# Optimization experiments

Hardware: AMD Instinct MI355X
Metric: run time of the kernel (lower is better)

The kernel has to match this reference:

```python
import jax, jax.numpy as jnp
import numpy as np
from jax import lax

B, T, NI = 1024, 16, 11

def skew(v):  # [...,3,1] -> [...,3,3]
    x, y, z = v[..., 0, 0], v[..., 1, 0], v[..., 2, 0]
    o = jnp.zeros_like(x)
    return jnp.stack([jnp.stack([o, -z, y], -1),
                      jnp.stack([z, o, -x], -1),
                      jnp.stack([-y, x, o], -1)], -2)

def exp_SO3(phi):  # [...,3,1] -> [...,3,3] (Rodrigues, safe small-angle)
    t2 = jnp.sum(phi * phi, axis=(-2, -1))[..., None, None]
    small = t2 < 1e-8
    t2s = jnp.where(small, 1.0, t2)
    t = jnp.sqrt(t2s)
    A = jnp.where(small, 1.0 - t2 / 6.0, jnp.sin(t) / t)
    Bc = jnp.where(small, 0.5 - t2 / 24.0, (1.0 - jnp.cos(t)) / t2s)
    K = skew(phi)
    return jnp.eye(3, dtype=phi.dtype) + A * K + Bc * (K @ K)

def log_SO3(C):  # [...,3,3] -> [...,3,1]
    tr = jnp.trace(C, axis1=-2, axis2=-1)[..., None, None]
    c = jnp.clip((tr - 1.0) * 0.5, -1.0 + 1e-7, 1.0 - 1e-7)
    t = jnp.arccos(c)
    small = t < 1e-4
    s = jnp.where(small, 1.0, jnp.sin(t))
    coef = jnp.where(small, 0.5 + t * t / 12.0, t / (2.0 * s))
    S = coef * (C - jnp.swapaxes(C, -1, -2))
    return jnp.stack([S[..., 2, 1], S[..., 0, 2], S[..., 1, 0]], -1)[..., None]

def J_left_inv(phi):  # inverse left Jacobian of SO(3)
    t2 = jnp.sum(phi * phi, axis=(-2, -1))[..., None, None]
    small = t2 < 1e-8
    t2s = jnp.where(small, 1.0, t2)
    t = jnp.sqrt(t2s)
    coef = jnp.where(small, 1.0 / 12.0,
                     1.0 / t2s - (1.0 + jnp.cos(t)) / (2.0 * t * jnp.sin(t)))
    K = skew(phi)
    return jnp.eye(3, dtype=phi.dtype) - 0.5 * K + coef * (K @ K)

def decode(s):
    b = s.shape[0]
    return (s[:, 0:3].reshape(b, 3, 1), s[:, 3:12].reshape(b, 3, 3),
            s[:, 12:15].reshape(b, 3, 1), s[:, 15:18].reshape(b, 3, 1),
            s[:, 18:21].reshape(b, 3, 1), s[:, 21:24].reshape(b, 3, 1),
            s[:, 24].reshape(b, 1, 1))

def encode(g, C, r, v, bw, ba, lambd):
    b = g.shape[0]
    return jnp.concatenate([g.reshape(b, 3), C.reshape(b, 9), r.reshape(b, 3),
                            v.reshape(b, 3), bw.reshape(b, 3), ba.reshape(b, 3),
                            lambd.reshape(b, 1)], -1)

def force_sym(M):
    u = jnp.triu(M)
    return u + jnp.swapaxes(u, -1, -2) * (1.0 - jnp.eye(M.shape[-1], dtype=M.dtype))

def predict_one_step(t_acc, C_acc, r_acc, v_acc, dt, g_k, v_k, bw_k, ba_k, covar, gyro, accel, Rimu):
    b = dt.shape[0]
    dt2 = dt * dt
    w = gyro - bw_k
    w_sk = skew(w)
    C_T = jnp.swapaxes(C_acc, -1, -2)
    a = accel - ba_k
    v = C_T @ (v_k - g_k * t_acc + v_acc)
    v_sk = skew(v)
    I3 = jnp.eye(3, dtype=dt.dtype)
    E = exp_SO3(dt * w)
    E_T = jnp.swapaxes(E, -1, -2)
    F = jnp.zeros((b, 19, 19), dt.dtype)
    F = F.at[:, 3:6, 3:6].set(-w_sk)
    F = F.at[:, 3:6, 12:15].set(-I3)
    F = F.at[:, 6:9, 3:6].set(-(C_acc @ v_sk))
    F = F.at[:, 6:9, 9:12].set(C_acc)
    F = F.at[:, 9:12, 0:3].set(-C_T)
    F = F.at[:, 9:12, 3:6].set(-skew(C_T @ g_k))
    F = F.at[:, 9:12, 9:12].set(-w_sk)
    F = F.at[:, 9:12, 12:15].set(-v_sk)
    F = F.at[:, 9:12, 15:18].set(-I3)
    G = jnp.zeros((b, 19, 12), dt.dtype)
    G = G.at[:, 3:6, 0:3].set(-I3)
    G = G.at[:, 9:12, 0:3].set(-v_sk)
    G = G.at[:, 9:12, 6:9].set(-I3)
    G = G.at[:, 12:15, 3:6].set(I3)
    G = G.at[:, 15:18, 9:12].set(I3)
    Phi = jnp.eye(19, dtype=dt.dtype) + F * dt + 0.5 * (F @ F) * dt2
    Phi = Phi.at[:, 6:9, 12:15].set(0.0)
    Phi = Phi.at[:, 3:6, 3:6].set(E_T)
    Phi = Phi.at[:, 9:12, 9:12].set(E_T)
    PhiG = Phi @ G
    Q = (PhiG @ Rimu @ jnp.swapaxes(PhiG, -1, -2)) * dt
    covar = force_sym(Phi @ covar @ jnp.swapaxes(Phi, -1, -2) + Q)
    r_acc = r_acc + v_acc * dt + 0.5 * (C_acc @ (dt2 * a))
    v_acc = v_acc + C_acc @ (dt * a)
    C_acc = C_acc @ E
    t_acc = t_acc + dt
    return t_acc, C_acc, r_acc, v_acc, covar

def predict(imu_meas, Rimu, prev_state, prev_covar):
    b = imu_meas.shape[0]
    dtype = prev_covar.dtype
    g_k, _, _, v_k, bw_k, ba_k, lambd = decode(prev_state)
    u = jnp.array([1.0] * 3 + [0.0] * 6 + [1.0] * 10, dtype)
    covar = prev_covar * (u[:, None] * u[None, :])  # U P U^T with diagonal U
    t = imu_meas[..., 0]
    gyro = imu_meas[..., 1:4][..., None]
    accel = imu_meas[..., 4:7][..., None]
    dt = (t[:, 1:] - t[:, :-1])[..., None, None]
    init = (jnp.zeros((b, 1, 1), dtype),
            jnp.tile(jnp.eye(3, dtype=dtype), (b, 1, 1)),
            jnp.zeros((b, 3, 1), dtype), jnp.zeros((b, 3, 1), dtype), covar)
    xs = (jnp.swapaxes(dt, 0, 1), jnp.swapaxes(gyro[:, :-1], 0, 1), jnp.swapaxes(accel[:, :-1], 0, 1))
    def step(c, x):
        t_acc, C_acc, r_acc, v_acc, cov = c
        dt_, gy, ac = x
        return predict_one_step(t_acc, C_acc, r_acc, v_acc, dt_, g_k, v_k, bw_k, ba_k, cov, gy, ac, Rimu), None
    (t_acc, C_acc, r_acc, v_acc, cov), _ = lax.scan(step, init, xs)
    pred_state = encode(g_k, C_acc,
                        v_k * t_acc - 0.5 * g_k * t_acc * t_acc + r_acc,
                        jnp.swapaxes(C_acc, -1, -2) @ (v_k - g_k * t_acc + v_acc),
                        bw_k, ba_k, lambd)
    return pred_state, cov

def update(pred_state, pred_covar, vis_meas, vis_meas_covar):
    b = pred_state.shape[0]
    dtype = pred_state.dtype
    g_p, C_p, r_p, v_p, bw_p, ba_p, l_p = decode(pred_state)
    phi = log_SO3(C_p)
    residual = jnp.concatenate([vis_meas[:, 0:3] - phi, vis_meas[:, 3:6] - l_p * r_p], 1)
    H = jnp.zeros((b, 6, 19), dtype)
    H = H.at[:, 0:3, 3:6].set(-J_left_inv(-phi))
    H = H.at[:, 3:6, 6:9].set(-jnp.eye(3, dtype=dtype) * l_p)
    H = H.at[:, 3:6, 18:19].set(-r_p)
    H = -H
    H_T = jnp.swapaxes(H, -1, -2)
    S = H @ pred_covar @ H_T + vis_meas_covar
    K = pred_covar @ H_T @ jnp.linalg.inv(S)
    e = K @ residual
    est_covar = (jnp.eye(19, dtype=dtype) - K @ H) @ pred_covar
    est_state = encode(g_p + e[:, 0:3], C_p @ exp_SO3(e[:, 3:6]), r_p + e[:, 6:9],
                       v_p + e[:, 9:12], bw_p + e[:, 12:15], ba_p + e[:, 15:18],
                       l_p + e[:, 18:19])
    return est_state, est_covar

def composition(prev_pose, est_state, est_covar):
    b = est_state.shape[0]
    dtype = est_state.dtype
    g, C, r, v, bw, ba, lambd = decode(est_state)
    C_T = jnp.swapaxes(C, -1, -2)
    pose = jnp.tile(jnp.eye(4, dtype=dtype), (b, 1, 1))
    pose = pose.at[:, 0:3, 0:3].set(C_T @ prev_pose[:, 0:3, 0:3])
    pose = pose.at[:, 0:3, 3:4].set(C_T @ (prev_pose[:, 0:3, 3:4] - r))
    new_g = C_T @ g
    new_state = encode(new_g, C, r, v, bw, ba, lambd)
    U = jnp.tile(jnp.eye(19, dtype=dtype), (b, 1, 1))
    U = U.at[:, 0:3, 0:3].set(C_T)
    U = U.at[:, 0:3, 3:6].set(skew(new_g))
    new_covar = force_sym(U @ est_covar @ jnp.swapaxes(U, -1, -2))
    return pose, new_state, new_covar

def setup_inputs() -> dict:
    key = jax.random.key(0)
    k1, k2, k3 = jax.random.split(key, 3)
    dtype = jnp.float32
    times = jnp.broadcast_to(jnp.arange(NI, dtype=dtype) * 0.01, (B, T, NI))
    gyro = jax.random.normal(k1, (B, T, NI, 3), dtype) * 0.05
    accel = jax.random.normal(k2, (B, T, NI, 3), dtype) * 0.1
    imu_data = jnp.concatenate([times[..., None], gyro, accel], -1)  # [B,T,NI,7]
    imu_noise_covar = jnp.eye(12, dtype=dtype) * 1e-4
    prev_pose = jnp.tile(jnp.eye(4, dtype=dtype), (B, 1, 1))
    g0 = jnp.array([0.0, 0.0, 9.81], dtype)
    C0 = jnp.eye(3, dtype=dtype).reshape(9)
    prev_state = jnp.broadcast_to(
        jnp.concatenate([g0, C0, jnp.zeros(12, dtype), jnp.ones(1, dtype)]), (B, 25))
    prev_covar = jnp.tile(jnp.eye(19, dtype=dtype) * 1e-2, (B, 1, 1))
    vis_meas = jax.random.normal(k3, (B, T, 6, 1), dtype) * 0.01
    vis_meas_covar = jnp.tile(jnp.eye(6, dtype=dtype) * 1e-2, (B, T, 1, 1))
    T_imu_cam = jnp.tile(jnp.eye(4, dtype=dtype), (B, 1, 1))
    return dict(imu_data=imu_data, imu_noise_covar=imu_noise_covar, prev_pose=prev_pose,
                prev_state=prev_state, prev_covar=prev_covar, vis_meas=vis_meas,
                vis_meas_covar=vis_meas_covar, T_imu_cam=T_imu_cam)

def reference(imu_data, imu_noise_covar, prev_pose, prev_state, prev_covar, vis_meas, vis_meas_covar, T_imu_cam):
    num_timesteps = vis_meas.shape[1]
    poses, states, covars = [prev_pose], [prev_state], [prev_covar]
    for k in range(num_timesteps):
        ps, pc = predict(imu_data[:, k], imu_noise_covar, states[-1], covars[-1])
        es, ec = update(ps, pc, vis_meas[:, k], vis_meas_covar[:, k])
        npo, ns, nc = composition(poses[-1], es, ec)
        poses.append(npo); states.append(ns); covars.append(nc)
    return (jnp.stack(poses, 1), jnp.stack(states, 1), jnp.stack(covars, 1))
```

## Files before the change

kernel.cpp:

```cpp
#include <hip/hip_runtime.h>

#define NB 1024
#define NT 16
#define NIM 11
#define PIT 20
#define NTH 256
#define TPF 128

struct __align__(16) SharedBlob {
    float P0[19*PIT];
    float P1[19*PIT];
    float A9[9*PIT];
    float Dall[10][9*PIT];
    float Wsall[10][9*12];
    float Wu[19*12];
    float Mu[19*12];
    float T[3*PIT];
    float Rd[12];
    float sqRd[12];
    float Aug[2][84];
    float E[20];
    float dts[12];
    unsigned short tri[192];
};

__device__ __forceinline__ float sel3(int i, float a, float b, float c){
    return i==0 ? a : (i==1 ? b : c);
}
__device__ __forceinline__ void skew3(float x, float y, float z, float K[9]) {
    K[0]=0.f;  K[1]=-z;   K[2]=y;
    K[3]=z;    K[4]=0.f;  K[5]=-x;
    K[6]=-y;   K[7]=x;    K[8]=0.f;
}
__device__ __forceinline__ void mm3(const float A[9], const float Bm[9], float C[9]) {
#pragma unroll
    for (int i=0;i<3;i++)
#pragma unroll
        for (int j=0;j<3;j++)
            C[i*3+j] = A[i*3+0]*Bm[0+j] + A[i*3+1]*Bm[3+j] + A[i*3+2]*Bm[6+j];
}
__device__ __forceinline__ void exp_SO3f(float p0, float p1, float p2, float R[9]) {
    float t2 = p0*p0+p1*p1+p2*p2;
    bool sm = t2 < 1e-8f;
    float t2s = sm ? 1.0f : t2;
    float t = sqrtf(t2s);
    float sn, cs; __sincosf(t, &sn, &cs);
    float A = sm ? (1.0f - t2*(1.0f/6.0f)) : (sn/t);
    float Bc = sm ? (0.5f - t2*(1.0f/24.0f)) : ((1.0f - cs)/t2s);
    float K[9]; skew3(p0,p1,p2,K);
    float K2[9]; mm3(K,K,K2);
#pragma unroll
    for (int i=0;i<9;i++) R[i] = A*K[i] + Bc*K2[i];
    R[0]+=1.f; R[4]+=1.f; R[8]+=1.f;
}
__device__ __forceinline__ void log_SO3(const float C[9], float p[3]) {
    float tr = C[0]+C[4]+C[8];
    float c = (tr-1.0f)*0.5f;
    c = fminf(fmaxf(c, -1.0f+1e-7f), 1.0f-1e-7f);
    float t = acosf(c);
    bool sm = t < 1e-4f;
    float s = sm ? 1.0f : sinf(t);
    float coef = sm ? (0.5f + t*t*(1.0f/12.0f)) : (t/(2.0f*s));
    p[0] = coef*(C[7]-C[5]);
    p[1] = coef*(C[2]-C[6]);
    p[2] = coef*(C[3]-C[1]);
}
__device__ __forceinline__ void J_left_inv(const float p[3], float J[9]) {
    float t2 = p[0]*p[0]+p[1]*p[1]+p[2]*p[2];
    bool sm = t2 < 1e-8f;
    float t2s = sm ? 1.0f : t2;
    float t = sqrtf(t2s);
    float coef = sm ? (1.0f/12.0f) : (1.0f/t2s - (1.0f+cosf(t))/(2.0f*t*sinf(t)));
    float K[9]; skew3(p[0],p[1],p[2],K);
    float K2[9]; mm3(K,K,K2);
#pragma unroll
    for (int i=0;i<9;i++) J[i] = -0.5f*K[i] + coef*K2[i];
    J[0]+=1.f; J[4]+=1.f; J[8]+=1.f;
}
__device__ __forceinline__ float dot19_rr(const float* a, const float* b){
    const float4* a4=(const float4*)a;
    const float4* b4=(const float4*)b;
    float s=0.f;
#pragma unroll
    for (int q=0;q<4;q++){
        float4 x=a4[q], y=b4[q];
        s += x.x*y.x + x.y*y.y + x.z*y.z + x.w*y.w;
    }
    s += a[16]*b[16]+a[17]*b[17]+a[18]*b[18];
    return s;
}
__device__ __forceinline__ float dot12_rr(const float* a, const float* b){
    const float4* a4=(const float4*)a;
    const float4* b4=(const float4*)b;
    float s=0.f;
#pragma unroll
    for (int q=0;q<3;q++){
        float4 x=a4[q], y=b4[q];
        s += x.x*y.x + x.y*y.y + x.z*y.z + x.w*y.w;
    }
    return s;
}

__global__ void __launch_bounds__(NTH, 2) kf_kernel(
    const float* __restrict__ imu_data,
    const float* __restrict__ Rimu,
    const float* __restrict__ prev_pose,
    const float* __restrict__ prev_state,
    const float* __restrict__ prev_covar,
    const float* __restrict__ vis_meas,
    const float* __restrict__ vis_covar,
    float* __restrict__ out_poses,
    float* __restrict__ out_states,
    float* __restrict__ out_covars)
{
    __shared__ SharedBlob SS[2];
    const int tid = threadIdx.x;
    const int f   = tid >> 7;
    const int t   = tid & (TPF-1);
    const int b   = blockIdx.x*2 + f;
    SharedBlob& S = SS[f];
    const int w = t >> 6;
    const int l = t & 63;

    const float* pcv = prev_covar + (size_t)b*361;
    for (int e=t;e<361;e+=TPF){
        float v = pcv[e];
        int i=e/19, j=e%19;
        bool msk = (i>=3&&i<9)||(j>=3&&j<9);
        S.P0[i*PIT + j] = msk ? 0.f : v;
        out_covars[((size_t)b*17)*361 + e] = v;
    }
    for (int e=t;e<10*9*PIT;e+=TPF) S.Dall[0][e] = 0.f;
    if (t<12){ float rv = Rimu[t*12+t]; S.Rd[t]=rv; S.sqRd[t]=sqrtf(rv); }
    if (t<16) out_poses[((size_t)b*17)*16 + t] = prev_pose[(size_t)b*16+t];
    if (t<25) out_states[((size_t)b*17)*25 + t] = prev_state[(size_t)b*25+t];
    for (int e=t;e<190;e+=TPF){
        int i=0, rem=e;
        while (rem >= 19-i){ rem -= 19-i; i++; }
        S.tri[e] = (unsigned short)((i<<5)|(i+rem));
    }

    const float* st = prev_state + (size_t)b*25;
    float g0=st[0], g1=st[1], g2=st[2];
    float vk0=st[15], vk1=st[16], vk2=st[17];
    float bw0=st[18], bw1=st[19], bw2=st[20];
    float ba0=st[21], ba1=st[22], ba2=st[23];
    float lam=st[24];
    const float* pp = prev_pose + (size_t)b*16;
    float pR[9] = {pp[0],pp[1],pp[2], pp[4],pp[5],pp[6], pp[8],pp[9],pp[10]};
    float pT0=pp[3], pT1=pp[7], pT2=pp[11];

    __syncthreads();

    for (int k=0;k<NT;k++){
        float Cc[9] = {1,0,0, 0,1,0, 0,0,1};
        float ra0=0,ra1=0,ra2=0, va0=0,va1=0,va2=0, tac=0;
        const float* imu = imu_data + ((size_t)b*NT + k)*NIM*7;

        for (int s=0;s<NIM-1;s++){
            const float* m0 = imu + s*7;
            float dt = m0[7] - m0[0];
            float w0=m0[1]-bw0, w1=m0[2]-bw1, w2=m0[3]-bw2;
            float a0=m0[4]-ba0, a1=m0[5]-ba1, a2=m0[6]-ba2;
            float u0=vk0-g0*tac+va0, u1=vk1-g1*tac+va1, u2=vk2-g2*tac+va2;
            float vv0=Cc[0]*u0+Cc[3]*u1+Cc[6]*u2;
            float vv1=Cc[1]*u0+Cc[4]*u1+Cc[7]*u2;
            float vv2=Cc[2]*u0+Cc[5]*u1+Cc[8]*u2;
            float ct0=Cc[0]*g0+Cc[3]*g1+Cc[6]*g2;
            float ct1=Cc[1]*g0+Cc[4]*g1+Cc[7]*g2;
            float ct2=Cc[2]*g0+Cc[5]*g1+Cc[8]*g2;
            float Em[9]; exp_SO3f(dt*w0, dt*w1, dt*w2, Em);
            float hdt2 = 0.5f*dt*dt;

            if (t<27){
                int r=t/9, ii=(t%9)/3, jj=t%3;
                float dij = (ii==jj)?1.f:0.f;
                int o = ii*PIT + jj;
                float* Dp = S.Dall[s];
                if (r==0){
                    float eJ0=sel3(jj,Em[0],Em[3],Em[6]), eJ1=sel3(jj,Em[1],Em[4],Em[7]), eJ2=sel3(jj,Em[2],Em[5],Em[8]);
                    float EmTIJ = sel3(ii,eJ0,eJ1,eJ2);
                    float wcJ0=sel3(jj,0.f,-w2,w1), wcJ1=sel3(jj,w2,0.f,-w0), wcJ2=sel3(jj,-w1,w0,0.f);
                    float wskIJ = sel3(ii,wcJ0,wcJ1,wcJ2);
                    Dp[o+3]  = EmTIJ - dij;
                    Dp[o+12] = -dt*dij + hdt2*wskIJ;
                } else if (r==1){
                    float cI0=sel3(ii,Cc[0],Cc[3],Cc[6]), cI1=sel3(ii,Cc[1],Cc[4],Cc[7]), cI2=sel3(ii,Cc[2],Cc[5],Cc[8]);
                    float cJ0=sel3(jj,Cc[0],Cc[3],Cc[6]), cJ1=sel3(jj,Cc[1],Cc[4],Cc[7]), cJ2=sel3(jj,Cc[2],Cc[5],Cc[8]);
                    float ccJ0=sel3(jj,Cc[0],Cc[1],Cc[2]), ccJ1=sel3(jj,Cc[3],Cc[4],Cc[5]), ccJ2=sel3(jj,Cc[6],Cc[7],Cc[8]);
                    float CIJ = sel3(ii,ccJ0,ccJ1,ccJ2);
                    float vcJ0=sel3(jj,0.f,-vv2,vv1), vcJ1=sel3(jj,vv2,0.f,-vv0), vcJ2=sel3(jj,-vv1,vv0,0.f);
                    float tcJ0=sel3(jj,0.f,-ct2,ct1), tcJ1=sel3(jj,ct2,0.f,-ct0), tcJ2=sel3(jj,-ct1,ct0,0.f);
                    float wcJ0=sel3(jj,0.f,-w2,w1), wcJ1=sel3(jj,w2,0.f,-w0), wcJ2=sel3(jj,-w1,w0,0.f);
                    float CCtIJ  = cI0*cJ0 + cI1*cJ1 + cI2*cJ2;
                    float CvskIJ = cI0*vcJ0 + cI1*vcJ1 + cI2*vcJ2;
                    float Cv0 =  cI1*vv2 - cI2*vv1;
                    float Cv1 = -cI0*vv2 + cI2*vv0;
                    float Cv2 =  cI0*vv1 - cI1*vv0;
                    float CvwIJ = Cv0*wcJ0 + Cv1*wcJ1 + Cv2*wcJ2;
                    float CctIJ = cI0*tcJ0 + cI1*tcJ1 + cI2*tcJ2;
                    float CwIJ  = cI0*wcJ0 + cI1*wcJ1 + cI2*wcJ2;
                    Dp[3*PIT + o + 0]  = -hdt2*CCtIJ;
                    Dp[3*PIT + o + 3]  = -dt*CvskIJ + hdt2*(CvwIJ - CctIJ);
                    Dp[3*PIT + o + 9]  =  dt*CIJ - hdt2*CwIJ;
                    Dp[3*PIT + o + 15] = -hdt2*CIJ;
                } else {
                    float cJ0=sel3(jj,Cc[0],Cc[3],Cc[6]), cJ1=sel3(jj,Cc[1],Cc[4],Cc[7]), cJ2=sel3(jj,Cc[2],Cc[5],Cc[8]);
                    float CTIJ = sel3(ii,cJ0,cJ1,cJ2);
                    float eJ0=sel3(jj,Em[0],Em[3],Em[6]), eJ1=sel3(jj,Em[1],Em[4],Em[7]), eJ2=sel3(jj,Em[2],Em[5],Em[8]);
                    float EmTIJ = sel3(ii,eJ0,eJ1,eJ2);
                    float wrI0=sel3(ii,0.f,w2,-w1), wrI1=sel3(ii,-w2,0.f,w0), wrI2=sel3(ii,w1,-w0,0.f);
                    float wcJ0=sel3(jj,0.f,-w2,w1), wcJ1=sel3(jj,w2,0.f,-w0), wcJ2=sel3(jj,-w1,w0,0.f);
                    float wskIJ = sel3(ii,wcJ0,wcJ1,wcJ2);
                    float vcJ0=sel3(jj,0.f,-vv2,vv1), vcJ1=sel3(jj,vv2,0.f,-vv0), vcJ2=sel3(jj,-vv1,vv0,0.f);
                    float vskIJ = sel3(ii,vcJ0,vcJ1,vcJ2);
                    float trI0=sel3(ii,0.f,ct2,-ct1), trI1=sel3(ii,-ct2,0.f,ct0), trI2=sel3(ii,ct1,-ct0,0.f);
                    float tcJ0=sel3(jj,0.f,-ct2,ct1), tcJ1=sel3(jj,ct2,0.f,-ct0), tcJ2=sel3(jj,-ct1,ct0,0.f);
                    float ctskIJ = sel3(ii,tcJ0,tcJ1,tcJ2);
                    float wCtIJ = wrI0*cJ0 + wrI1*cJ1 + wrI2*cJ2;
                    float ctwIJ = trI0*wcJ0 + trI1*wcJ1 + trI2*wcJ2;
                    float wctIJ = wrI0*tcJ0 + wrI1*tcJ1 + wrI2*tcJ2;
                    float wvIJ  = wrI0*vcJ0 + wrI1*vcJ1 + wrI2*vcJ2;
                    Dp[6*PIT + o + 0]  = -dt*CTIJ + hdt2*wCtIJ;
                    Dp[6*PIT + o + 3]  = -dt*ctskIJ + hdt2*(ctwIJ + wctIJ);
                    Dp[6*PIT + o + 9]  = EmTIJ - dij;
                    Dp[6*PIT + o + 12] = -dt*vskIJ + hdt2*(ctskIJ + wvIJ);
                    Dp[6*PIT + o + 15] = -dt*dij + hdt2*wskIJ;
                }
            }
            if (t==3) S.dts[s] = dt;
            if (w==0){
                __builtin_amdgcn_wave_barrier();
                asm volatile("s_waitcnt lgkmcnt(0)" ::: "memory");
                __builtin_amdgcn_wave_barrier();
                float* Wp = S.Wsall[s];
                const float* Dp2 = S.Dall[s];
                for (int e=l;e<108;e+=64){
                    int i=e/12, j=e%12;
                    const float* Dr = &Dp2[i*PIT];
                    int ri = 3+i;
                    float val;
                    if (j<3){
                        float v0j = sel3(j, 0.f, -vv2,  vv1);
                        float v1j = sel3(j, vv2,  0.f, -vv0);
                        float v2j = sel3(j,-vv1,  vv0,  0.f);
                        val = -((ri==3+j)?1.f:0.f) - Dr[3+j]
                              - (((ri==9 )?1.f:0.f)+Dr[9 ])*v0j
                              - (((ri==10)?1.f:0.f)+Dr[10])*v1j
                              - (((ri==11)?1.f:0.f)+Dr[11])*v2j;
                    } else if (j<6) val = Dr[9+j];
                    else if (j<9) val = -(((ri==j+3)?1.f:0.f) + Dr[j+3]);
                    else val = Dr[6+j];
                    Wp[i*12+j] = val * S.sqRd[j];
                }
            }

            float d2 = dt*dt;
            float e0=d2*a0, e1=d2*a1, e2=d2*a2;
            ra0 += va0*dt + 0.5f*(Cc[0]*e0+Cc[1]*e1+Cc[2]*e2);
            ra1 += va1*dt + 0.5f*(Cc[3]*e0+Cc[4]*e1+Cc[5]*e2);
            ra2 += va2*dt + 0.5f*(Cc[6]*e0+Cc[7]*e1+Cc[8]*e2);
            float da0=dt*a0, da1=dt*a1, da2=dt*a2;
            va0 += Cc[0]*da0+Cc[1]*da1+Cc[2]*da2;
            va1 += Cc[3]*da0+Cc[4]*da1+Cc[5]*da2;
            va2 += Cc[6]*da0+Cc[7]*da1+Cc[8]*da2;
            float Cn[9]; mm3(Cc, Em, Cn);
#pragma unroll
            for (int q=0;q<9;q++) Cc[q]=Cn[q];
            tac += dt;
        }
        __syncthreads();

        for (int s=0;s<NIM-1;s++){
            float* Pc = (s&1) ? S.P1 : S.P0;
            float* Pn = (s&1) ? S.P0 : S.P1;
            const float* Ds = S.Dall[s];
            const float* Wss = S.Wsall[s];
            float dt = S.dts[s];

            int aBeg = (w==0)?0:57, aEnd = (w==0)?57:171;
            for (int e=aBeg+l;e<aEnd;e+=64){
                int i=e/19, j=e%19;
                const float* Dr = &Ds[i*PIT];
                float s2 = Pc[(3+i)*PIT+j]
                         + Dr[0]*Pc[0*PIT+j]+Dr[1]*Pc[1*PIT+j]+Dr[2]*Pc[2*PIT+j]
                         + Dr[3]*Pc[3*PIT+j]+Dr[4]*Pc[4*PIT+j]+Dr[5]*Pc[5*PIT+j]
                         + Dr[9]*Pc[9*PIT+j]+Dr[10]*Pc[10*PIT+j]+Dr[11]*Pc[11*PIT+j]
                         + Dr[12]*Pc[12*PIT+j]+Dr[13]*Pc[13*PIT+j]+Dr[14]*Pc[14*PIT+j]
                         + Dr[15]*Pc[15*PIT+j]+Dr[16]*Pc[16*PIT+j]+Dr[17]*Pc[17*PIT+j];
                S.A9[i*PIT+j]=s2;
            }
            __builtin_amdgcn_wave_barrier();
            asm volatile("s_waitcnt lgkmcnt(0)" ::: "memory");
            __builtin_amdgcn_wave_barrier();

            int tBase = (w==0)?0:99, tCnt = (w==0)?99:91;
            for (int e2=l;e2<tCnt;e2+=64){
                int tt=S.tri[tBase+e2]; int i=tt>>5, j=tt&31;
                const float* Ai = (i>=3 && i<12) ? &S.A9[(i-3)*PIT] : &Pc[i*PIT];
                float val = Ai[j];
                if (j>=3 && j<12) val += dot19_rr(Ai, &Ds[(j-3)*PIT]);
                if (i>=3){
                    if (j<12) val += dt*dot12_rr(&Wss[(i-3)*12], &Wss[(j-3)*12]);
                    else if (i<12){
                        if (j<15) val += dt*Wss[(i-3)*12 + (j-9)]*S.sqRd[j-9];
                        else if (j<18) val += dt*Wss[(i-3)*12 + (j-6)]*S.sqRd[j-6];
                    } else if (i==j){
                        if (i<15) val += dt*S.Rd[i-9];
                        else if (i<18) val += dt*S.Rd[i-6];
                    }
                }
                Pn[i*PIT+j]=val; Pn[j*PIT+i]=val;
            }
            __syncthreads();
        }

        float t2a = tac*tac;
        float rp0 = vk0*tac - 0.5f*g0*t2a + ra0;
        float rp1 = vk1*tac - 0.5f*g1*t2a + ra1;
        float rp2 = vk2*tac - 0.5f*g2*t2a + ra2;
        float u0=vk0-g0*tac+va0, u1=vk1-g1*tac+va1, u2=vk2-g2*tac+va2;
        float vpr0=Cc[0]*u0+Cc[3]*u1+Cc[6]*u2;
        float vpr1=Cc[1]*u0+Cc[4]*u1+Cc[7]*u2;
        float vpr2=Cc[2]*u0+Cc[5]*u1+Cc[8]*u2;

        float phi[3]; log_SO3(Cc, phi);
        float nphi[3]={-phi[0],-phi[1],-phi[2]};
        float Jli[9]; J_left_inv(nphi, Jli);
        const float* vm = vis_meas + ((size_t)b*NT+k)*6;
        float res0=vm[0]-phi[0], res1=vm[1]-phi[1], res2=vm[2]-phi[2];
        float res3=vm[3]-lam*rp0, res4=vm[4]-lam*rp1, res5=vm[5]-lam*rp2;

        if (t<114){
            int i=t/6, j=t%6;
            float val;
            if (j<3){
                float jr0 = sel3(j, Jli[0], Jli[3], Jli[6]);
                float jr1 = sel3(j, Jli[1], Jli[4], Jli[7]);
                float jr2 = sel3(j, Jli[2], Jli[5], Jli[8]);
                val = S.P0[i*PIT+3]*jr0 + S.P0[i*PIT+4]*jr1 + S.P0[i*PIT+5]*jr2;
            } else {
                float rsel = sel3(j-3, rp0, rp1, rp2);
                val = lam*S.P0[i*PIT+6+(j-3)] + rsel*S.P0[i*PIT+18];
            }
            S.Wu[i*12+j]=val;
        }
        __syncthreads();
        const float* vmc = vis_covar + ((size_t)b*NT+k)*36;
        if (t<84){
            int i=t/14, c=t%14;
            float val;
            if (c<6){
                float hp;
                if (i<3){
                    float jr0 = sel3(i, Jli[0], Jli[3], Jli[6]);
                    float jr1 = sel3(i, Jli[1], Jli[4], Jli[7]);
                    float jr2 = sel3(i, Jli[2], Jli[5], Jli[8]);
                    hp = jr0*S.Wu[3*12+c]+jr1*S.Wu[4*12+c]+jr2*S.Wu[5*12+c];
                } else {
                    float rsel = sel3(i-3, rp0, rp1, rp2);
                    hp = lam*S.Wu[(3+i)*12+c] + rsel*S.Wu[18*12+c];
                }
                val = hp + vmc[i*6+c];
            } else val = ((c-6)==i)?1.f:0.f;
            S.Aug[0][i*14+c]=val;
        }
        __syncthreads();
        if (t<64){
            int i0=t/14, c0=t%14;
            int e1=t+64, i1=e1/14, c1=e1%14;
            bool h1 = e1<84;
            int cur=0;
#pragma unroll
            for (int kk=0;kk<6;kk++){
                const float* Ac = S.Aug[cur];
                float* An = S.Aug[cur^1];
                float rpv = 1.0f/Ac[kk*14+kk];
                float piv0 = Ac[kk*14+c0]*rpv;
                float nv0 = (i0==kk)? piv0 : (Ac[i0*14+c0] - Ac[i0*14+kk]*piv0);
                float nv1 = 0.f;
                if (h1){
                    float piv1 = Ac[kk*14+c1]*rpv;
                    nv1 = (i1==kk)? piv1 : (Ac[i1*14+c1] - Ac[i1*14+kk]*piv1);
                }
                An[i0*14+c0]=nv0;
                if (h1) An[i1*14+c1]=nv1;
                cur^=1;
                __builtin_amdgcn_wave_barrier();
            }
        }
        __syncthreads();
        if (t<114){
            int i=t/6, j=t%6;
            float s2=0.f;
#pragma unroll
            for (int m=0;m<6;m++) s2 += S.Wu[i*12+m]*S.Aug[0][m*14+6+j];
            S.Mu[i*12+j]=s2;
        }
        __syncthreads();
        for (int e=t;e<133;e+=TPF){
            int i=e/7, c=e%7;
            float val;
            if (c<3){
                float jc0 = sel3(c, Jli[0], Jli[1], Jli[2]);
                float jc1 = sel3(c, Jli[3], Jli[4], Jli[5]);
                float jc2 = sel3(c, Jli[6], Jli[7], Jli[8]);
                val = S.Mu[i*12+0]*jc0 + S.Mu[i*12+1]*jc1 + S.Mu[i*12+2]*jc2;
            }
            else if (c<6) val = S.Mu[i*12+c]*lam;
            else val = S.Mu[i*12+3]*rp0 + S.Mu[i*12+4]*rp1 + S.Mu[i*12+5]*rp2;
            S.Wu[i*12+c]=val;
        }
        if (t<19){
            S.E[t] = S.Mu[t*12+0]*res0 + S.Mu[t*12+1]*res1 + S.Mu[t*12+2]*res2
                   + S.Mu[t*12+3]*res3 + S.Mu[t*12+4]*res4 + S.Mu[t*12+5]*res5;
        }
        __syncthreads();
        for (int e=t;e<361;e+=TPF){
            int i=e/19, j=e%19;
            float s2 = S.P0[i*PIT+j];
#pragma unroll
            for (int c=0;c<6;c++) s2 -= S.Wu[i*12+c]*S.P0[(3+c)*PIT+j];
            s2 -= S.Wu[i*12+6]*S.P0[18*PIT+j];
            S.P1[i*PIT+j]=s2;
        }
        float ev[19];
#pragma unroll
        for (int q=0;q<19;q++) ev[q]=S.E[q];
        g0+=ev[0]; g1+=ev[1]; g2+=ev[2];
        float dE[9]; exp_SO3f(ev[3], ev[4], ev[5], dE);
        float Ce[9]; mm3(Cc,dE,Ce);
        float re0=rp0+ev[6], re1=rp1+ev[7], re2=rp2+ev[8];
        float vE0=vpr0+ev[9], vE1=vpr1+ev[10], vE2=vpr2+ev[11];
        bw0+=ev[12]; bw1+=ev[13]; bw2+=ev[14];
        ba0+=ev[15]; ba1+=ev[16]; ba2+=ev[17];
        lam+=ev[18];
        float gn0=Ce[0]*g0+Ce[3]*g1+Ce[6]*g2;
        float gn1=Ce[1]*g0+Ce[4]*g1+Ce[7]*g2;
        float gn2=Ce[2]*g0+Ce[5]*g1+Ce[8]*g2;
        float Rn[9];
#pragma unroll
        for (int i=0;i<3;i++)
#pragma unroll
            for (int j=0;j<3;j++)
                Rn[i*3+j] = Ce[0*3+i]*pR[0*3+j] + Ce[1*3+i]*pR[1*3+j] + Ce[2*3+i]*pR[2*3+j];
        float dv0=pT0-re0, dv1=pT1-re1, dv2=pT2-re2;
        float Tn0=Ce[0]*dv0+Ce[3]*dv1+Ce[6]*dv2;
        float Tn1=Ce[1]*dv0+Ce[4]*dv1+Ce[7]*dv2;
        float Tn2=Ce[2]*dv0+Ce[5]*dv1+Ce[8]*dv2;
        __syncthreads();
        if (t<57){
            int i=t/19, j=t%19;
            float c0 = sel3(i, Ce[0], Ce[1], Ce[2]);
            float c1 = sel3(i, Ce[3], Ce[4], Ce[5]);
            float c2 = sel3(i, Ce[6], Ce[7], Ce[8]);
            float gs0 = sel3(i, 0.f,  gn2, -gn1);
            float gs1 = sel3(i, -gn2, 0.f,  gn0);
            float gs2 = sel3(i, gn1, -gn0,  0.f);
            float val = c0*S.P1[0*PIT+j] + c1*S.P1[1*PIT+j] + c2*S.P1[2*PIT+j]
                      + gs0*S.P1[3*PIT+j] + gs1*S.P1[4*PIT+j] + gs2*S.P1[5*PIT+j];
            S.T[i*PIT+j]=val;
        }
        __syncthreads();
        size_t obase = (size_t)b*17 + (size_t)(k+1);
        for (int e=t;e<190;e+=TPF){
            int tt=S.tri[e]; int i=tt>>5, j=tt&31;
            float val;
            if (j<3){
                float c0 = sel3(j, Ce[0], Ce[1], Ce[2]);
                float c1 = sel3(j, Ce[3], Ce[4], Ce[5]);
                float c2 = sel3(j, Ce[6], Ce[7], Ce[8]);
                float gs0 = sel3(j, 0.f,  gn2, -gn1);
                float gs1 = sel3(j, -gn2, 0.f,  gn0);
                float gs2 = sel3(j, gn1, -gn0,  0.f);
                val = S.T[i*PIT+0]*c0 + S.T[i*PIT+1]*c1 + S.T[i*PIT+2]*c2
                    + S.T[i*PIT+3]*gs0 + S.T[i*PIT+4]*gs1 + S.T[i*PIT+5]*gs2;
            } else {
                val = (i<3) ? S.T[i*PIT+j] : S.P1[i*PIT+j];
            }
            bool msk = (i>=3&&i<9)||(j>=3&&j<9);
            float pv = msk ? 0.f : val;
            S.P0[i*PIT+j]=pv; S.P0[j*PIT+i]=pv;
            out_covars[obase*361 + i*19 + j] = val;
            if (i!=j) out_covars[obase*361 + j*19 + i] = val;
        }
        if (t==0){
            float* po = out_poses + obase*16;
            po[0]=Rn[0]; po[1]=Rn[1]; po[2]=Rn[2];  po[3]=Tn0;
            po[4]=Rn[3]; po[5]=Rn[4]; po[6]=Rn[5];  po[7]=Tn1;
            po[8]=Rn[6]; po[9]=Rn[7]; po[10]=Rn[8]; po[11]=Tn2;
            po[12]=0.f; po[13]=0.f; po[14]=0.f; po[15]=1.f;
            float* so = out_states + obase*25;
            so[0]=gn0; so[1]=gn1; so[2]=gn2;
#pragma unroll
            for (int q=0;q<9;q++) so[3+q]=Ce[q];
            so[12]=re0; so[13]=re1; so[14]=re2;
            so[15]=vE0; so[16]=vE1; so[17]=vE2;
            so[18]=bw0; so[19]=bw1; so[20]=bw2;
            so[21]=ba0; so[22]=ba1; so[23]=ba2;
            so[24]=lam;
        }
        g0=gn0; g1=gn1; g2=gn2;
        vk0=vE0; vk1=vE1; vk2=vE2;
#pragma unroll
        for (int q=0;q<9;q++) pR[q]=Rn[q];
        pT0=Tn0; pT1=Tn1; pT2=Tn2;
        __syncthreads();
    }
}

extern "C" void kernel_launch(void* const* d_in, const int* in_sizes, int n_in,
                              void* d_out, int out_size, void* d_ws, size_t ws_size,
                              hipStream_t stream) {
    const float* imu    = (const float*)d_in[0];
    const float* Rimu   = (const float*)d_in[1];
    const float* ppose  = (const float*)d_in[2];
    const float* pstate = (const float*)d_in[3];
    const float* pcov   = (const float*)d_in[4];
    const float* vm     = (const float*)d_in[5];
    const float* vmc    = (const float*)d_in[6];
    float* out = (float*)d_out;
    float* out_poses  = out;
    float* out_states = out + (size_t)NB*17*16;
    float* out_covars = out + (size_t)NB*17*16 + (size_t)NB*17*25;
    hipLaunchKernelGGL(kf_kernel, dim3(NB/2), dim3(NTH), 0, stream,
        imu, Rimu, ppose, pstate, pcov, vm, vmc, out_poses, out_states, out_covars);
}
```

Measured before the change: 633.2 us.

## Restructure Kalman update stage to cut block-wide barriers

Builds the innovation matrix S directly from P0 in the same pass that computes P·Hᵀ, so the barrier between the two stages goes away. The residual is appended as an extra column of the augmented matrix so Gauss-Jordan elimination yields S⁻¹r. The H-projection of S⁻¹ (S⁻¹H) is computed inside the single-wave elimination block, and one product then gives the Kalman-gain-times-H and the state correction together. This removes about three block-wide __syncthreads per timestep, at the cost of redundant P·Hᵀ recomputation per augmented-matrix entry.

```diff
diff --git a/kernel.cpp b/kernel.cpp
--- a/kernel.cpp
+++ b/kernel.cpp
@@ -330,40 +330,54 @@
         const float* vm = vis_meas + ((size_t)b*NT+k)*6;
         float res0=vm[0]-phi[0], res1=vm[1]-phi[1], res2=vm[2]-phi[2];
         float res3=vm[3]-lam*rp0, res4=vm[4]-lam*rp1, res5=vm[5]-lam*rp2;
-
-        if (t<114){
-            int i=t/6, j=t%6;
-            float val;
-            if (j<3){
-                float jr0 = sel3(j, Jli[0], Jli[3], Jli[6]);
-                float jr1 = sel3(j, Jli[1], Jli[4], Jli[7]);
-                float jr2 = sel3(j, Jli[2], Jli[5], Jli[8]);
-                val = S.P0[i*PIT+3]*jr0 + S.P0[i*PIT+4]*jr1 + S.P0[i*PIT+5]*jr2;
+        const float* vmc = vis_covar + ((size_t)b*NT+k)*36;
+
+        for (int e=t;e<198;e+=TPF){
+            if (e<114){
+                int i=e/6, j=e%6;
+                float val;
+                if (j<3){
+                    float jr0 = sel3(j, Jli[0], Jli[3], Jli[6]);
+                    float jr1 = sel3(j, Jli[1], Jli[4], Jli[7]);
+                    float jr2 = sel3(j, Jli[2], Jli[5], Jli[8]);
+                    val = S.P0[i*PIT+3]*jr0 + S.P0[i*PIT+4]*jr1 + S.P0[i*PIT+5]*jr2;
+                } else {
+                    float rsel = sel3(j-3, rp0, rp1, rp2);
+                    val = lam*S.P0[i*PIT+6+(j-3)] + rsel*S.P0[i*PIT+18];
+                }
+                S.Wu[i*12+j]=val;
             } else {
-                float rsel = sel3(j-3, rp0, rp1, rp2);
-                val = lam*S.P0[i*PIT+6+(j-3)] + rsel*S.P0[i*PIT+18];
-            }
-            S.Wu[i*12+j]=val;
-        }
-        __syncthreads();
-        const float* vmc = vis_covar + ((size_t)b*NT+k)*36;
-        if (t<84){
-            int i=t/14, c=t%14;
-            float val;
-            if (c<6){
-                float hp;
-                if (i<3){
-                    float jr0 = sel3(i, Jli[0], Jli[3], Jli[6]);
-                    float jr1 = sel3(i, Jli[1], Jli[4], Jli[7]);
-                    float jr2 = sel3(i, Jli[2], Jli[5], Jli[8]);
-                    hp = jr0*S.Wu[3*12+c]+jr1*S.Wu[4*12+c]+jr2*S.Wu[5*12+c];
-                } else {
-                    float rsel = sel3(i-3, rp0, rp1, rp2);
-                    hp = lam*S.Wu[(3+i)*12+c] + rsel*S.Wu[18*12+c];
-                }
-                val = hp + vmc[i*6+c];
-            } else val = ((c-6)==i)?1.f:0.f;
-            S.Aug[0][i*14+c]=val;
+                int e2=e-114; int i=e2/14, c=e2%14;
+                float val;
+                if (c<6){
+                    auto phtv = [&](int row)->float {
+                        if (c<3){
+                            float j0=sel3(c,Jli[0],Jli[3],Jli[6]);
+                            float j1=sel3(c,Jli[1],Jli[4],Jli[7]);
+                            float j2=sel3(c,Jli[2],Jli[5],Jli[8]);
+                            return S.P0[row*PIT+3]*j0 + S.P0[row*PIT+4]*j1 + S.P0[row*PIT+5]*j2;
+                        } else {
+                            float rs=sel3(c-3,rp0,rp1,rp2);
+                            return lam*S.P0[row*PIT+6+(c-3)] + rs*S.P0[row*PIT+18];
+                        }
+                    };
+                    float hv;
+                    if (i<3){
+                        float a0=phtv(3), a1=phtv(4), a2=phtv(5);
+                        float j0=sel3(i,Jli[0],Jli[3],Jli[6]);
+                        float j1=sel3(i,Jli[1],Jli[4],Jli[7]);
+                        float j2=sel3(i,Jli[2],Jli[5],Jli[8]);
+                        hv = j0*a0 + j1*a1 + j2*a2;
+                    } else {
+                        float rs=sel3(i-3,rp0,rp1,rp2);
+                        hv = lam*phtv(6+(i-3)) + rs*phtv(18);
+                    }
+                    val = hv + vmc[i*6+c];
+                } else if (c<12) val = ((c-6)==i)?1.f:0.f;
+                else if (c==12) val = (i<3)? sel3(i,res0,res1,res2) : sel3(i-3,res3,res4,res5);
+                else val = 0.f;
+                S.Aug[0][i*14+c]=val;
+            }
         }
         __syncthreads();
         if (t<64){
@@ -388,40 +402,45 @@
                 cur^=1;
                 __builtin_amdgcn_wave_barrier();
             }
-        }
-        __syncthreads();
-        if (t<114){
-            int i=t/6, j=t%6;
-            float s2=0.f;
-#pragma unroll
-            for (int m=0;m<6;m++) s2 += S.Wu[i*12+m]*S.Aug[0][m*14+6+j];
-            S.Mu[i*12+j]=s2;
-        }
-        __syncthreads();
-        for (int e=t;e<133;e+=TPF){
-            int i=e/7, c=e%7;
-            float val;
-            if (c<3){
-                float jc0 = sel3(c, Jli[0], Jli[1], Jli[2]);
-                float jc1 = sel3(c, Jli[3], Jli[4], Jli[5]);
-                float jc2 = sel3(c, Jli[6], Jli[7], Jli[8]);
-                val = S.Mu[i*12+0]*jc0 + S.Mu[i*12+1]*jc1 + S.Mu[i*12+2]*jc2;
-            }
-            else if (c<6) val = S.Mu[i*12+c]*lam;
-            else val = S.Mu[i*12+3]*rp0 + S.Mu[i*12+4]*rp1 + S.Mu[i*12+5]*rp2;
-            S.Wu[i*12+c]=val;
-        }
-        if (t<19){
-            S.E[t] = S.Mu[t*12+0]*res0 + S.Mu[t*12+1]*res1 + S.Mu[t*12+2]*res2
-                   + S.Mu[t*12+3]*res3 + S.Mu[t*12+4]*res4 + S.Mu[t*12+5]*res5;
+            asm volatile("s_waitcnt lgkmcnt(0)" ::: "memory");
+            __builtin_amdgcn_wave_barrier();
+            if (t<42){
+                int m=t/7, c=t%7;
+                const float* Si = &S.Aug[0][m*14+6];
+                float val;
+                if (c<3){
+                    float j0=sel3(c,Jli[0],Jli[1],Jli[2]);
+                    float j1=sel3(c,Jli[3],Jli[4],Jli[5]);
+                    float j2=sel3(c,Jli[6],Jli[7],Jli[8]);
+                    val = Si[0]*j0 + Si[1]*j1 + Si[2]*j2;
+                } else if (c<6) val = lam*Si[c];
+                else val = Si[3]*rp0 + Si[4]*rp1 + Si[5]*rp2;
+                S.Aug[1][m*7+c] = val;
+            }
+        }
+        __syncthreads();
+        for (int e=t;e<152;e+=TPF){
+            if (e<133){
+                int i=e/7, c=e%7;
+                float s2=0.f;
+#pragma unroll
+                for (int m=0;m<6;m++) s2 += S.Wu[i*12+m]*S.Aug[1][m*7+c];
+                S.Mu[i*12+c]=s2;
+            } else {
+                int i=e-133;
+                float s2=0.f;
+#pragma unroll
+                for (int m=0;m<6;m++) s2 += S.Wu[i*12+m]*S.Aug[0][m*14+12];
+                S.E[i]=s2;
+            }
         }
         __syncthreads();
         for (int e=t;e<361;e+=TPF){
             int i=e/19, j=e%19;
             float s2 = S.P0[i*PIT+j];
 #pragma unroll
-            for (int c=0;c<6;c++) s2 -= S.Wu[i*12+c]*S.P0[(3+c)*PIT+j];
-            s2 -= S.Wu[i*12+6]*S.P0[18*PIT+j];
+            for (int c=0;c<6;c++) s2 -= S.Mu[i*12+c]*S.P0[(3+c)*PIT+j];
+            s2 -= S.Mu[i*12+6]*S.P0[18*PIT+j];
             S.P1[i*PIT+j]=s2;
         }
         float ev[19];
```

After: 642.4 us. About the same (+1.4%).
